# Kernel tuning notes

Measured on AMD Instinct MI355X. Metric: run time of the kernel, lower is better.

The kernel has to match this reference:

```python
import jax, jax.numpy as jnp
import numpy as np

B, C, H, W, K = 32, 64, 112, 112, 5


def setup_inputs() -> dict:
    key = jax.random.key(0)
    kx, = jax.random.split(key, 1)
    x = jax.random.uniform(kx, (B, C, H, W), dtype=jnp.float32)
    # parameters per BioNorm.reset_parameters()
    sigma = jnp.ones((C,), jnp.float32)
    pow_p = jnp.full((C,), 2.0, jnp.float32)
    sum_kernel = jnp.full((C, 1, K, K), 1.0 / (K * K), jnp.float32)
    weight = jnp.ones((C,), jnp.float32)
    bias = jnp.zeros((C,), jnp.float32)
    return {"x": x, "sigma": sigma, "pow_p": pow_p, "sum_kernel": sum_kernel,
            "weight": weight, "bias": bias}


def _bionorm(x, sigma, pow_p, sum_kernel, weight, bias):
    s = sigma.reshape(1, -1, 1, 1)
    p = pow_p.reshape(1, -1, 1, 1)
    w = weight.reshape(1, -1, 1, 1)
    b = bias.reshape(1, -1, 1, 1)
    xp = x ** p  # [B,C,H,W]
    # depthwise (grouped) conv, VALID padding -> [B,C,H-K+1,W-K+1]
    sf = jax.lax.conv_general_dilated(
        xp, sum_kernel, window_strides=(1, 1), padding='VALID',
        feature_group_count=C,
        dimension_numbers=('NCHW', 'OIHW', 'NCHW'))
    hks = K // 2
    # replicate-pad back to [B,C,H,W]
    sf = jnp.pad(sf, ((0, 0), (0, 0), (hks, hks), (hks, hks)), mode='edge')
    den = s ** p + sf
    return w * xp / den + b


def reference(x, sigma, pow_p, sum_kernel, weight, bias):
    return _bionorm(x, sigma, pow_p, sum_kernel, weight, bias)
```

## Files before the change

### kernel.cpp

```cpp
#include <hip/hip_runtime.h>


#define Cch 64
#define Hh 112
#define Ww 112
#define TH 28
#define LROWS (TH + 4)
#define ST 116

__global__ __launch_bounds__(256) void bionorm_kernel(
    const float* __restrict__ x, const float* __restrict__ sigma,
    const float* __restrict__ pow_p, const float* __restrict__ sum_kernel,
    const float* __restrict__ weight, const float* __restrict__ bias,
    float* __restrict__ out)
{
    __shared__ float lds[LROWS * ST];

    const int rt  = blockIdx.x;
    const int c   = blockIdx.y;
    const int b   = blockIdx.z;
    const int tid = threadIdx.x;
    const int r0  = rt * TH;

    const float p  = pow_p[c];
    const float sg = sigma[c];
    const float wc = weight[c];
    const float bc = bias[c];
    const bool  p2 = (p == 2.0f);
    const float sp = p2 ? sg * sg : __powf(sg, p);

    float kw[25];
    const float* kp = sum_kernel + c * 25;
    #pragma unroll
    for (int j = 0; j < 25; ++j) kw[j] = kp[j];

    const float* xplane = x + ((size_t)(b * Cch + c)) * Hh * Ww;

    for (int i = tid; i < LROWS * 28; i += 256) {
        int s = i / 28, q = i - s * 28;
        int g = r0 - 2 + s;
        g = g < 0 ? 0 : (g > 111 ? 111 : g);
        const float4 v = *(const float4*)(xplane + g * Ww + q * 4);
        float4 xp;
        if (p2) {
            xp.x = v.x * v.x; xp.y = v.y * v.y;
            xp.z = v.z * v.z; xp.w = v.w * v.w;
        } else {
            xp.x = __powf(v.x, p); xp.y = __powf(v.y, p);
            xp.z = __powf(v.z, p); xp.w = __powf(v.w, p);
        }
        *(float4*)(&lds[s * ST + q * 4]) = xp;
    }
    __syncthreads();

    float* oplane = out + ((size_t)(b * Cch + c)) * Hh * Ww;

    for (int i = tid; i < TH * 28; i += 256) {
        int lr = i / 28, gq = i - lr * 28;
        int r  = r0 + lr;
        int w0 = gq * 4;

        int cr    = r  < 2 ? 2 : (r  > 109 ? 109 : r);
        int cwmin = w0 < 2 ? 2 : (w0 > 109 ? 109 : w0);
        int base  = cwmin - 2;
        int sRow  = cr - r0;

        float S0 = 0.f, S1 = 0.f, S2 = 0.f, S3 = 0.f;
        #pragma unroll
        for (int dy = 0; dy < 5; ++dy) {
            const float* row = &lds[(sRow + dy) * ST + base];
            float rv[8];
            #pragma unroll
            for (int t = 0; t < 8; ++t) rv[t] = row[t];
            #pragma unroll
            for (int dx = 0; dx < 5; ++dx) {
                float kv = kw[dy * 5 + dx];
                S0 = fmaf(kv, rv[dx + 0], S0);
                S1 = fmaf(kv, rv[dx + 1], S1);
                S2 = fmaf(kv, rv[dx + 2], S2);
                S3 = fmaf(kv, rv[dx + 3], S3);
            }
        }

        const float4 xp4 = *(const float4*)(&lds[(lr + 2) * ST + w0]);
        const float xv[4] = {xp4.x, xp4.y, xp4.z, xp4.w};

        float res[4];
        #pragma unroll
        for (int j = 0; j < 4; ++j) {
            int wj  = w0 + j;
            int cwj = wj < 2 ? 2 : (wj > 109 ? 109 : wj);
            int off = cwj - cwmin;
            float s_ = off == 0 ? S0 : off == 1 ? S1 : off == 2 ? S2 : S3;
            res[j] = fmaf(wc * xv[j], __builtin_amdgcn_rcpf(sp + s_), bc);
        }
        float4 o = {res[0], res[1], res[2], res[3]};
        *(float4*)(oplane + r * Ww + w0) = o;
    }
}

extern "C" void kernel_launch(void* const* d_in, const int* in_sizes, int n_in,
                              void* d_out, int out_size, void* d_ws, size_t ws_size,
                              hipStream_t stream) {
    const float* x          = (const float*)d_in[0];
    const float* sigma      = (const float*)d_in[1];
    const float* pow_p      = (const float*)d_in[2];
    const float* sum_kernel = (const float*)d_in[3];
    const float* weight     = (const float*)d_in[4];
    const float* bias       = (const float*)d_in[5];
    float* out = (float*)d_out;

    dim3 grid(4, Cch, 32);
    dim3 block(256);
    bionorm_kernel<<<grid, block, 0, stream>>>(x, sigma, pow_p, sum_kernel,
                                               weight, bias, out);
}
```

Baseline: 214.7 us.

## Use register sliding window over conv rows and retile blocks to valid-output strips

Each thread now owns a 4-column strip and walks 9 consecutive conv-output rows, keeping a 5-row register window so each LDS row is loaded once instead of five times. Blocks are retiled into 3 strips of 36 valid rows with 128 threads, and edge replication is done by writing border rows and columns from the same registers. This cuts LDS traffic and index clamping, but uses more registers, idles 5 lanes per wave, and writes output as float2 instead of float4.

After: 202.6 us. -5.6%, faster.

```diff
diff --git a/kernel.cpp b/kernel.cpp
--- a/kernel.cpp
+++ b/kernel.cpp
@@ -4,23 +4,23 @@
 #define Cch 64
 #define Hh 112
 #define Ww 112
-#define TH 28
-#define LROWS (TH + 4)
 #define ST 116
+#define SROWS 40
+#define CPB 36
+#define RPS 9
 
-__global__ __launch_bounds__(256) void bionorm_kernel(
+__global__ __launch_bounds__(128) void bionorm_kernel(
     const float* __restrict__ x, const float* __restrict__ sigma,
     const float* __restrict__ pow_p, const float* __restrict__ sum_kernel,
     const float* __restrict__ weight, const float* __restrict__ bias,
     float* __restrict__ out)
 {
-    __shared__ float lds[LROWS * ST];
+    __shared__ float lds[SROWS * ST];
 
-    const int rt  = blockIdx.x;
+    const int bx  = blockIdx.x;
     const int c   = blockIdx.y;
     const int b   = blockIdx.z;
     const int tid = threadIdx.x;
-    const int r0  = rt * TH;
 
     const float p  = pow_p[c];
     const float sg = sigma[c];
@@ -34,13 +34,12 @@
     #pragma unroll
     for (int j = 0; j < 25; ++j) kw[j] = kp[j];
 
-    const float* xplane = x + ((size_t)(b * Cch + c)) * Hh * Ww;
+    const float* xplane = x + ((size_t)(b * Cch + c)) * (Hh * Ww);
+    const int r0 = bx * CPB;
 
-    for (int i = tid; i < LROWS * 28; i += 256) {
+    for (int i = tid; i < SROWS * 28; i += 128) {
         int s = i / 28, q = i - s * 28;
-        int g = r0 - 2 + s;
-        g = g < 0 ? 0 : (g > 111 ? 111 : g);
-        const float4 v = *(const float4*)(xplane + g * Ww + q * 4);
+        const float4 v = *(const float4*)(xplane + (r0 + s) * Ww + q * 4);
         float4 xp;
         if (p2) {
             xp.x = v.x * v.x; xp.y = v.y * v.y;
@@ -53,50 +52,74 @@
     }
     __syncthreads();
 
-    float* oplane = out + ((size_t)(b * Cch + c)) * Hh * Ww;
+    const int ss = tid >> 5;
+    const int g  = tid & 31;
+    if (g >= 27) return;
 
-    for (int i = tid; i < TH * 28; i += 256) {
-        int lr = i / 28, gq = i - lr * 28;
-        int r  = r0 + lr;
-        int w0 = gq * 4;
+    const int cs   = 2 + bx * CPB + ss * RPS;
+    const int col0 = 4 * g;
+    const int lbase = (9 * ss) * ST + col0;
 
-        int cr    = r  < 2 ? 2 : (r  > 109 ? 109 : r);
-        int cwmin = w0 < 2 ? 2 : (w0 > 109 ? 109 : w0);
-        int base  = cwmin - 2;
-        int sRow  = cr - r0;
+    float* oplane = out + ((size_t)(b * Cch + c)) * (Hh * Ww);
+
+    float win[5][8];
+
+    #define LOADW(SL, KR) { \
+        const float4 a_  = *(const float4*)(&lds[lbase + (KR) * ST]);     \
+        const float4 b_  = *(const float4*)(&lds[lbase + (KR) * ST + 4]); \
+        win[SL][0] = a_.x; win[SL][1] = a_.y; win[SL][2] = a_.z; win[SL][3] = a_.w; \
+        win[SL][4] = b_.x; win[SL][5] = b_.y; win[SL][6] = b_.z; win[SL][7] = b_.w; }
+
+    #define EMITROW(GR, SL) { \
+        float* orw_ = oplane + (GR) * Ww; \
+        *(float2*)(orw_ + col0 + 2) = make_float2(fmaf(wc * win[SL][2], d0, bc), \
+                                                  fmaf(wc * win[SL][3], d1, bc)); \
+        *(float2*)(orw_ + col0 + 4) = make_float2(fmaf(wc * win[SL][4], d2, bc), \
+                                                  fmaf(wc * win[SL][5], d3, bc)); \
+        if (g == 0)  *(float2*)(orw_)       = make_float2(fmaf(wc * win[SL][0], d0, bc), \
+                                                          fmaf(wc * win[SL][1], d0, bc)); \
+        if (g == 26) *(float2*)(orw_ + 110) = make_float2(fmaf(wc * win[SL][6], d3, bc), \
+                                                          fmaf(wc * win[SL][7], d3, bc)); }
+
+    LOADW(0, 0) LOADW(1, 1) LOADW(2, 2) LOADW(3, 3)
+
+    #pragma unroll
+    for (int k = 0; k < RPS; ++k) {
+        LOADW((k + 4) % 5, k + 4)
 
         float S0 = 0.f, S1 = 0.f, S2 = 0.f, S3 = 0.f;
         #pragma unroll
         for (int dy = 0; dy < 5; ++dy) {
-            const float* row = &lds[(sRow + dy) * ST + base];
-            float rv[8];
-            #pragma unroll
-            for (int t = 0; t < 8; ++t) rv[t] = row[t];
+            const int sl = (k + dy) % 5;
             #pragma unroll
             for (int dx = 0; dx < 5; ++dx) {
-                float kv = kw[dy * 5 + dx];
-                S0 = fmaf(kv, rv[dx + 0], S0);
-                S1 = fmaf(kv, rv[dx + 1], S1);
-                S2 = fmaf(kv, rv[dx + 2], S2);
-                S3 = fmaf(kv, rv[dx + 3], S3);
+                const float kv = kw[dy * 5 + dx];
+                S0 = fmaf(kv, win[sl][dx + 0], S0);
+                S1 = fmaf(kv, win[sl][dx + 1], S1);
+                S2 = fmaf(kv, win[sl][dx + 2], S2);
+                S3 = fmaf(kv, win[sl][dx + 3], S3);
             }
         }
 
-        const float4 xp4 = *(const float4*)(&lds[(lr + 2) * ST + w0]);
-        const float xv[4] = {xp4.x, xp4.y, xp4.z, xp4.w};
+        const float d0 = __builtin_amdgcn_rcpf(sp + S0);
+        const float d1 = __builtin_amdgcn_rcpf(sp + S1);
+        const float d2 = __builtin_amdgcn_rcpf(sp + S2);
+        const float d3 = __builtin_amdgcn_rcpf(sp + S3);
 
-        float res[4];
-        #pragma unroll
-        for (int j = 0; j < 4; ++j) {
-            int wj  = w0 + j;
-            int cwj = wj < 2 ? 2 : (wj > 109 ? 109 : wj);
-            int off = cwj - cwmin;
-            float s_ = off == 0 ? S0 : off == 1 ? S1 : off == 2 ? S2 : S3;
-            res[j] = fmaf(wc * xv[j], __builtin_amdgcn_rcpf(sp + s_), bc);
+        const int cgl = cs + k;
+        EMITROW(cgl, (k + 2) % 5)
+
+        if (cgl == 2) {
+            EMITROW(0, (k + 0) % 5)
+            EMITROW(1, (k + 1) % 5)
         }
-        float4 o = {res[0], res[1], res[2], res[3]};
-        *(float4*)(oplane + r * Ww + w0) = o;
+        if (cgl == 109) {
+            EMITROW(110, (k + 3) % 5)
+            EMITROW(111, (k + 4) % 5)
+        }
     }
+    #undef LOADW
+    #undef EMITROW
 }
 
 extern "C" void kernel_launch(void* const* d_in, const int* in_sizes, int n_in,
@@ -110,8 +133,8 @@
     const float* bias       = (const float*)d_in[5];
     float* out = (float*)d_out;
 
-    dim3 grid(4, Cch, 32);
-    dim3 block(256);
+    dim3 grid(3, Cch, 32);
+    dim3 block(128);
     bionorm_kernel<<<grid, block, 0, stream>>>(x, sigma, pow_p, sum_kernel,
                                                weight, bias, out);
 }
```

## Add uniform-kernel fast path with separable sliding box sum and realigned column groups

Applied to the files above, without the earlier changes.

Adds a runtime check for whether all 25 kernel weights are equal. When they are, the 5x5 convolution becomes column sums followed by a sliding horizontal window, scaled once by the shared weight. Columns are also remapped so each thread produces the 4 interior outputs at base+2..base+5 using aligned float4 LDS loads, with edge threads writing the replicate-padded borders. The general kernel path uses the same layout, which removes the per-element clamp selection, at the cost of extra branching and slightly different floating-point summation order.

Result: faster. 192.1 us (-10.5%).

```diff
diff --git a/kernel.cpp b/kernel.cpp
--- a/kernel.cpp
+++ b/kernel.cpp
@@ -5,7 +5,7 @@
 #define Hh 112
 #define Ww 112
 #define TH 28
-#define LROWS (TH + 4)
+#define LROWS 32
 #define ST 116
 
 __global__ __launch_bounds__(256) void bionorm_kernel(
@@ -33,8 +33,11 @@
     const float* kp = sum_kernel + c * 25;
     #pragma unroll
     for (int j = 0; j < 25; ++j) kw[j] = kp[j];
+    bool uni = true;
+    #pragma unroll
+    for (int j = 1; j < 25; ++j) uni = uni && (kw[j] == kw[0]);
 
-    const float* xplane = x + ((size_t)(b * Cch + c)) * Hh * Ww;
+    const float* xplane = x + ((size_t)(b * Cch + c)) * (Hh * Ww);
 
     for (int i = tid; i < LROWS * 28; i += 256) {
         int s = i / 28, q = i - s * 28;
@@ -53,50 +56,106 @@
     }
     __syncthreads();
 
-    float* oplane = out + ((size_t)(b * Cch + c)) * Hh * Ww;
+    float* oplane = out + ((size_t)(b * Cch + c)) * (Hh * Ww);
 
-    for (int i = tid; i < TH * 28; i += 256) {
-        int lr = i / 28, gq = i - lr * 28;
-        int r  = r0 + lr;
-        int w0 = gq * 4;
+    #define STOREOUT() { \
+        float* orw_ = oplane + r * Ww; \
+        *(float2*)(orw_ + base + 2) = make_float2(fmaf(wc * n2, d0, bc), \
+                                                  fmaf(wc * n3, d1, bc)); \
+        *(float2*)(orw_ + base + 4) = make_float2(fmaf(wc * n4, d2, bc), \
+                                                  fmaf(wc * n5, d3, bc)); \
+        if (g == 0)  *(float2*)(orw_)       = make_float2(fmaf(wc * n0, d0, bc), \
+                                                          fmaf(wc * n1, d0, bc)); \
+        if (g == 26) *(float2*)(orw_ + 110) = make_float2(fmaf(wc * n6, d3, bc), \
+                                                          fmaf(wc * n7, d3, bc)); }
 
-        int cr    = r  < 2 ? 2 : (r  > 109 ? 109 : r);
-        int cwmin = w0 < 2 ? 2 : (w0 > 109 ? 109 : w0);
-        int base  = cwmin - 2;
-        int sRow  = cr - r0;
+    #define RENUM() { \
+        if (r != cr) {  \
+            const float* nrw_ = &lds[(lr + 2) * ST + base]; \
+            const float4 na_ = *(const float4*)(nrw_); \
+            const float4 nb_ = *(const float4*)(nrw_ + 4); \
+            n0 = na_.x; n1 = na_.y; n2 = na_.z; n3 = na_.w; \
+            n4 = nb_.x; n5 = nb_.y; n6 = nb_.z; n7 = nb_.w; } }
 
-        float S0 = 0.f, S1 = 0.f, S2 = 0.f, S3 = 0.f;
-        #pragma unroll
-        for (int dy = 0; dy < 5; ++dy) {
-            const float* row = &lds[(sRow + dy) * ST + base];
-            float rv[8];
+    if (uni) {
+        const float k0 = kw[0];
+        for (int i = tid; i < TH * 27; i += 256) {
+            const int lr = i / 27, g = i - lr * 27;
+            const int r    = r0 + lr;
+            const int cr   = r < 2 ? 2 : (r > 109 ? 109 : r);
+            const int sRow = cr - r0;
+            const int base = 4 * g;
+
+            float v0 = 0.f, v1 = 0.f, v2 = 0.f, v3 = 0.f;
+            float v4 = 0.f, v5 = 0.f, v6 = 0.f, v7 = 0.f;
+            float n0, n1, n2, n3, n4, n5, n6, n7;
             #pragma unroll
-            for (int t = 0; t < 8; ++t) rv[t] = row[t];
+            for (int dy = 0; dy < 5; ++dy) {
+                const float* row = &lds[(sRow + dy) * ST + base];
+                const float4 a = *(const float4*)(row);
+                const float4 e = *(const float4*)(row + 4);
+                v0 += a.x; v1 += a.y; v2 += a.z; v3 += a.w;
+                v4 += e.x; v5 += e.y; v6 += e.z; v7 += e.w;
+                if (dy == 2) {
+                    n0 = a.x; n1 = a.y; n2 = a.z; n3 = a.w;
+                    n4 = e.x; n5 = e.y; n6 = e.z; n7 = e.w;
+                }
+            }
+            RENUM()
+
+            const float h0 = ((v0 + v1) + (v2 + v3)) + v4;
+            const float h1 = h0 - v0 + v5;
+            const float h2 = h1 - v1 + v6;
+            const float h3 = h2 - v2 + v7;
+
+            const float d0 = __builtin_amdgcn_rcpf(fmaf(k0, h0, sp));
+            const float d1 = __builtin_amdgcn_rcpf(fmaf(k0, h1, sp));
+            const float d2 = __builtin_amdgcn_rcpf(fmaf(k0, h2, sp));
+            const float d3 = __builtin_amdgcn_rcpf(fmaf(k0, h3, sp));
+
+            STOREOUT()
+        }
+    } else {
+        for (int i = tid; i < TH * 27; i += 256) {
+            const int lr = i / 27, g = i - lr * 27;
+            const int r    = r0 + lr;
+            const int cr   = r < 2 ? 2 : (r > 109 ? 109 : r);
+            const int sRow = cr - r0;
+            const int base = 4 * g;
+
+            float S0 = 0.f, S1 = 0.f, S2 = 0.f, S3 = 0.f;
+            float n0, n1, n2, n3, n4, n5, n6, n7;
             #pragma unroll
-            for (int dx = 0; dx < 5; ++dx) {
-                float kv = kw[dy * 5 + dx];
-                S0 = fmaf(kv, rv[dx + 0], S0);
-                S1 = fmaf(kv, rv[dx + 1], S1);
-                S2 = fmaf(kv, rv[dx + 2], S2);
-                S3 = fmaf(kv, rv[dx + 3], S3);
+            for (int dy = 0; dy < 5; ++dy) {
+                const float* row = &lds[(sRow + dy) * ST + base];
+                const float4 a = *(const float4*)(row);
+                const float4 e = *(const float4*)(row + 4);
+                const float rv[8] = {a.x, a.y, a.z, a.w, e.x, e.y, e.z, e.w};
+                #pragma unroll
+                for (int dx = 0; dx < 5; ++dx) {
+                    const float kv = kw[dy * 5 + dx];
+                    S0 = fmaf(kv, rv[dx + 0], S0);
+                    S1 = fmaf(kv, rv[dx + 1], S1);
+                    S2 = fmaf(kv, rv[dx + 2], S2);
+                    S3 = fmaf(kv, rv[dx + 3], S3);
+                }
+                if (dy == 2) {
+                    n0 = rv[0]; n1 = rv[1]; n2 = rv[2]; n3 = rv[3];
+                    n4 = rv[4]; n5 = rv[5]; n6 = rv[6]; n7 = rv[7];
+                }
             }
+            RENUM()
+
+            const float d0 = __builtin_amdgcn_rcpf(sp + S0);
+            const float d1 = __builtin_amdgcn_rcpf(sp + S1);
+            const float d2 = __builtin_amdgcn_rcpf(sp + S2);
+            const float d3 = __builtin_amdgcn_rcpf(sp + S3);
+
+            STOREOUT()
         }
-
-        const float4 xp4 = *(const float4*)(&lds[(lr + 2) * ST + w0]);
-        const float xv[4] = {xp4.x, xp4.y, xp4.z, xp4.w};
-
-        float res[4];
-        #pragma unroll
-        for (int j = 0; j < 4; ++j) {
-            int wj  = w0 + j;
-            int cwj = wj < 2 ? 2 : (wj > 109 ? 109 : wj);
-            int off = cwj - cwmin;
-            float s_ = off == 0 ? S0 : off == 1 ? S1 : off == 2 ? S2 : S3;
-            res[j] = fmaf(wc * xv[j], __builtin_amdgcn_rcpf(sp + s_), bc);
-        }
-        float4 o = {res[0], res[1], res[2], res[3]};
-        *(float4*)(oplane + r * Ww + w0) = o;
     }
+    #undef STOREOUT
+    #undef RENUM
 }
 
 extern "C" void kernel_launch(void* const* d_in, const int* in_sizes, int n_in,
```
